# Performance work log

Measured on AMD Instinct MI355X. Metric: run time of the kernel, lower is better.

## Reference

```python
import jax, jax.numpy as jnp
import numpy as np

B, T, H = 32, 4096, 128   # batch, seq len, feature dim (ctor L=128)
N = 128                    # S5 state size (S5(dim, dim))
DEPTH = 2                  # L_LT
D_OUT = 64                 # adaptive pool output length (ctor D)
LN_EPS = 1e-5


def setup_inputs() -> dict:
    key = jax.random.key(0)
    ks = iter(jax.random.split(key, 40))
    def nrm(shape, s):
        return (jax.random.normal(next(ks), shape, jnp.float32) * s).astype(jnp.float32)
    inp = {}
    inp['x'] = jax.random.normal(next(ks), (B, T, H), jnp.float32)
    # LayerNorm params (stacked over depth)
    inp['ln1_g'] = jnp.ones((DEPTH, H), jnp.float32)
    inp['ln1_b'] = jnp.zeros((DEPTH, H), jnp.float32)
    inp['ln2_g'] = jnp.ones((DEPTH, H), jnp.float32)
    inp['ln2_b'] = jnp.zeros((DEPTH, H), jnp.float32)
    # S5 params: diagonal complex Lambda, complex B/C, real D skip, per-state log step
    inp['Lam_re'] = -0.5 * jnp.ones((DEPTH, N), jnp.float32)
    inp['Lam_im'] = jnp.tile(jnp.pi * jnp.arange(N, dtype=jnp.float32), (DEPTH, 1))
    inp['B_re'] = nrm((DEPTH, N, H), 1.0 / np.sqrt(H))
    inp['B_im'] = nrm((DEPTH, N, H), 1.0 / np.sqrt(H))
    inp['C_re'] = nrm((DEPTH, H, N), 1.0 / np.sqrt(N))
    inp['C_im'] = nrm((DEPTH, H, N), 1.0 / np.sqrt(N))
    inp['D_skip'] = nrm((DEPTH, H), 1.0)
    inp['log_step'] = jax.random.uniform(next(ks), (DEPTH, N), jnp.float32,
                                         minval=np.log(1e-3), maxval=np.log(1e-1))
    # MLP params
    inp['W1'] = nrm((DEPTH, H, 2 * H), 1.0 / np.sqrt(H))
    inp['b1'] = jnp.zeros((DEPTH, 2 * H), jnp.float32)
    inp['W2'] = nrm((DEPTH, 2 * H, H), 1.0 / np.sqrt(2 * H))
    inp['b2'] = jnp.zeros((DEPTH, H), jnp.float32)
    # Conv1d params (out_ch, in_ch, k=5)
    cs = 1.0 / np.sqrt(H * 5)
    inp['conv1_w'] = nrm((H, H, 5), cs)
    inp['conv1_b'] = jnp.zeros((H,), jnp.float32)
    inp['conv2_w'] = nrm((H, H, 5), cs)
    inp['conv2_b'] = jnp.zeros((H,), jnp.float32)
    return inp


def _layer_norm(x, g, b):
    mu = jnp.mean(x, axis=-1, keepdims=True)
    var = jnp.mean(jnp.square(x - mu), axis=-1, keepdims=True)
    return (x - mu) * jax.lax.rsqrt(var + LN_EPS) * g + b


def _s5(u, lam_re, lam_im, b_re, b_im, c_re, c_im, d_skip, log_step):
    # u: [B, T, H] real. Diagonal S5 with ZOH discretization + parallel scan.
    lam = lam_re + 1j * lam_im                       # (N,) complex
    dt = jnp.exp(log_step)                           # (N,)
    lam_bar = jnp.exp(lam * dt)                      # (N,)
    Bc = b_re + 1j * b_im                            # (N, H)
    B_bar = ((lam_bar - 1.0) / lam)[:, None] * Bc    # (N, H)
    Bu = jnp.einsum('bth,nh->btn', u.astype(jnp.complex64), B_bar)  # [B,T,N]
    A = jnp.broadcast_to(lam_bar.astype(jnp.complex64), Bu.shape)
    def binop(e1, e2):
        a1, x1 = e1
        a2, x2 = e2
        return a1 * a2, a2 * x1 + x2
    _, xs = jax.lax.associative_scan(binop, (A, Bu), axis=1)        # [B,T,N]
    Cc = c_re + 1j * c_im                            # (H, N)
    y = 2.0 * jnp.real(jnp.einsum('btn,hn->bth', xs, Cc)) + u * d_skip
    return y


def _conv1d_s2(x, w, b):
    # x: [B, C, L]; stride 2, padding 2, kernel 5
    y = jax.lax.conv_general_dilated(x, w, window_strides=(2,), padding=[(2, 2)],
                                     dimension_numbers=('NCH', 'OIH', 'NCH'))
    return y + b[None, :, None]


def reference(x, ln1_g, ln1_b, ln2_g, ln2_b, Lam_re, Lam_im, B_re, B_im,
              C_re, C_im, D_skip, log_step, W1, b1, W2, b2,
              conv1_w, conv1_b, conv2_w, conv2_b):
    for i in range(DEPTH):
        # S5 sub-block
        res = x
        xn = _layer_norm(x, ln1_g[i], ln1_b[i])
        x = res + _s5(xn, Lam_re[i], Lam_im[i], B_re[i], B_im[i],
                      C_re[i], C_im[i], D_skip[i], log_step[i])
        # MLP sub-block (dropout = identity in eval)
        res = x
        xn = _layer_norm(x, ln2_g[i], ln2_b[i])
        h = jax.nn.gelu(jnp.einsum('bth,hf->btf', xn, W1[i]) + b1[i], approximate=False)
        x = res + jnp.einsum('btf,fh->bth', h, W2[i]) + b2[i]
    x = jnp.transpose(x, (0, 2, 1))                  # [B, H, T]
    x = jax.nn.relu(_conv1d_s2(x, conv1_w, conv1_b))  # [B, H, T/2]
    x = jax.nn.relu(_conv1d_s2(x, conv2_w, conv2_b))  # [B, H, T/4]
    Lin = x.shape[-1]
    # AdaptiveAvgPool1d(D_OUT): Lin divisible by D_OUT -> uniform windows
    x = x.reshape(x.shape[0], x.shape[1], D_OUT, Lin // D_OUT).mean(axis=-1)
    return x  # [B, H, D_OUT]
```

## Files before the change

### kernel.cpp

```cpp
#include <hip/hip_runtime.h>
#include <math.h>

#define BATCH 32
#define TSEQ  4096
#define HD    128
#define NST   128
#define BT    (BATCH*TSEQ)
#define LC    64
#define NCHK  (TSEQ/LC)

typedef unsigned short bf16;
typedef __attribute__((ext_vector_type(8))) short bf16x8;
typedef __attribute__((ext_vector_type(4))) float f32x4;

__device__ inline float bf2f(bf16 s) {
    union { unsigned int u; float f; } v; v.u = ((unsigned int)s) << 16; return v.f;
}
__device__ inline bf16 f2bf(float f) {
    union { float f; unsigned int u; } v; v.f = f;
    unsigned int u = v.u;
    unsigned int r = (u + 0x7fffu + ((u >> 16) & 1u)) >> 16;
    return (bf16)r;
}
__device__ inline unsigned int pkpair(float lo, float hi) {
    union { float f; unsigned int u; } a, b;
    a.f = lo; b.f = hi;
    return __builtin_amdgcn_perm(b.u + 0x8000u, a.u + 0x8000u, 0x07060302u);
}
__device__ inline bf16x8 pack8f(float4 f0, float4 f1) {
    union { bf16x8 v; unsigned int u[4]; } t;
    t.u[0] = pkpair(f0.x, f0.y);
    t.u[1] = pkpair(f0.z, f0.w);
    t.u[2] = pkpair(f1.x, f1.y);
    t.u[3] = pkpair(f1.z, f1.w);
    return t.v;
}
__device__ inline float2 cmul2(float2 a, float2 b) {
    return make_float2(a.x*b.x - a.y*b.y, a.x*b.y + a.y*b.x);
}
__device__ inline float gelu_f(float x) {
    float u = x*(0.7978845608f + 0.0356774081f*x*x);
    return __fdividef(x, 1.f + __expf(-2.f*u));
}
__device__ inline float2 upk(unsigned int w) {
    union { unsigned int u; float f; } a, b;
    a.u = w << 16; b.u = w & 0xffff0000u;
    return make_float2(a.f, b.f);
}
__device__ inline unsigned int pk(float2 x) { return pkpair(x.x, x.y); }

__global__ void prep_s5(const float* __restrict__ Lam_re, const float* __restrict__ Lam_im,
                        const float* __restrict__ B_re,  const float* __restrict__ B_im,
                        const float* __restrict__ C_re,  const float* __restrict__ C_im,
                        const float* __restrict__ log_step,
                        const float* __restrict__ ln1_g, const float* __restrict__ ln1_b,
                        const float* __restrict__ D_skip,
                        bf16* __restrict__ Wbu_bf,
                        bf16* __restrict__ Wc_bf,
                        float* __restrict__ Sb, float* __restrict__ biasb,
                        float* __restrict__ gd, float* __restrict__ bd,
                        float4* __restrict__ coefs,
                        float2* __restrict__ apow)
{
    int i = blockIdx.x, n = threadIdx.x;
    int in = i*NST + n;
    float lr = Lam_re[in], li = Lam_im[in];
    float dt = expf(log_step[in]);
    float ea = expf(lr*dt);
    float ar = ea*cosf(li*dt), ai = ea*sinf(li*dt);
    float xx = ar - 1.f, yy = ai;
    float den = lr*lr + li*li;
    float sr = (xx*lr + yy*li)/den;
    float si = (yy*lr - xx*li)/den;
    float2 a2 = make_float2(ar, ai);
    float2 p = a2;
    float2* apr = apow + (size_t)i*64*128;
    for (int j = 0; j < 64; ++j) {
        apr[j*128 + n] = p;
        p = cmul2(p, a2);
    }
    float2 q = a2;
    #pragma unroll
    for (int t = 0; t < 6; ++t) q = cmul2(q, q);
    coefs[in] = make_float4(ar, ai, q.x, q.y);

    const float* g  = ln1_g + i*HD;
    const float* bb = ln1_b + i*HD;
    const float* br = B_re + (size_t)in*HD;
    const float* bi = B_im + (size_t)in*HD;
    bf16* wb = Wbu_bf + (size_t)i*256*128;
    float s_re = 0.f, s_im = 0.f, bc_re = 0.f, bc_im = 0.f;
    for (int h = 0; h < HD; ++h) {
        float wre = sr*br[h] - si*bi[h];
        float wim = sr*bi[h] + si*br[h];
        bf16 wrb = f2bf(g[h]*wre), wib = f2bf(g[h]*wim);
        wb[(2*n)*128 + h]   = wrb;
        wb[(2*n+1)*128 + h] = wib;
        s_re += bf2f(wrb); s_im += bf2f(wib);
        bc_re += bb[h]*wre; bc_im += bb[h]*wim;
    }
    Sb[i*256 + 2*n] = s_re;     Sb[i*256 + 2*n+1] = s_im;
    biasb[i*256 + 2*n] = bc_re; biasb[i*256 + 2*n+1] = bc_im;

    const float* cr = C_re + (size_t)i*HD*NST;
    const float* ci = C_im + (size_t)i*HD*NST;
    bf16* wc = Wc_bf + (size_t)i*128*256;
    for (int h = 0; h < HD; ++h) {
        wc[h*256 + 2*n]   = f2bf( 2.f * cr[h*NST + n]);
        wc[h*256 + 2*n+1] = f2bf(-2.f * ci[h*NST + n]);
    }
    gd[i*HD + n] = g[n]*D_skip[i*HD + n];
    bd[i*HD + n] = bb[n]*D_skip[i*HD + n];
}

__global__ void prep_w1(const float* __restrict__ W1, const float* __restrict__ b1,
                        const float* __restrict__ ln2_g, const float* __restrict__ ln2_b,
                        bf16* __restrict__ W1_bf, float* __restrict__ S1,
                        float* __restrict__ bias1p)
{
    int i = blockIdx.x, f = threadIdx.x;
    const float* g  = ln2_g + i*HD;
    const float* bb = ln2_b + i*HD;
    bf16* w = W1_bf + (size_t)i*256*128;
    float S = 0.f, bi_ = b1[i*256 + f];
    for (int h = 0; h < HD; ++h) {
        float wv = W1[(size_t)i*32768 + h*256 + f];
        bf16 wbv = f2bf(g[h]*wv);
        w[f*128 + h] = wbv;
        S += bf2f(wbv);
        bi_ += bb[h]*wv;
    }
    S1[i*256 + f] = S;
    bias1p[i*256 + f] = bi_;
}

__global__ void prep_w2(const float* __restrict__ W2, bf16* __restrict__ W2_bf)
{
    int i = blockIdx.x, h = threadIdx.x;
    bf16* w = W2_bf + (size_t)i*128*256;
    for (int f = 0; f < 256; ++f)
        w[h*256 + f] = f2bf(W2[(size_t)i*32768 + f*128 + h]);
}

__global__ void prep_wB(const float* __restrict__ w1, const float* __restrict__ w2,
                        bf16* __restrict__ wB1, bf16* __restrict__ wB2)
{
    int idx = blockIdx.x*256 + threadIdx.x;
    if (idx >= 163840) return;
    const float* w = (idx < 81920) ? w1 : w2;
    bf16* wb       = (idx < 81920) ? wB1 : wB2;
    int r   = idx % 81920;
    int c   = r / 640;
    int tap = (r % 640) / 128;
    int ic  = r % 128;
    wb[r] = f2bf(w[(c*128 + ic)*5 + tap]);
}

template<int UD, typename TA>
__global__ __launch_bounds__(1024, 4) void lngemm(
    const TA* __restrict__ A,
    const bf16* __restrict__ Bt,
    const float* __restrict__ Svec, const float* __restrict__ bvec,
    bf16* __restrict__ outB,
    float2* __restrict__ munrs)
{
    __shared__ bf16 Bs[256*136];
    __shared__ float Sl[256], bl[256];

    int tid = threadIdx.x;
    #pragma unroll
    for (int it = 0; it < 4; ++it) {
        int f = it*1024 + tid;
        int n = f >> 4, kk = (f & 15)*8;
        *(bf16x8*)&Bs[n*136 + kk] = *(const bf16x8*)(Bt + n*128 + kk);
    }
    if (tid < 256) { Sl[tid] = Svec[tid]; bl[tid] = bvec[tid]; }
    __syncthreads();

    int wid = tid >> 6, lane = tid & 63;
    int quad = lane >> 4, cl = lane & 15;
    int s = blockIdx.x*16 + wid;
    size_t row = (size_t)s*16 + cl;

    bf16x8 af[4];
    float sm = 0.f, sq = 0.f;
    if constexpr (sizeof(TA) == 2) {
        const bf16* ar = (const bf16*)A + row*128;
        #pragma unroll
        for (int ks = 0; ks < 4; ++ks) {
            af[ks] = *(const bf16x8*)(ar + quad*8 + ks*32);
            union { bf16x8 v; unsigned int u[4]; } aa; aa.v = af[ks];
            #pragma unroll
            for (int jp = 0; jp < 4; ++jp) {
                float2 vv = upk(aa.u[jp]);
                sm += vv.x + vv.y;
                sq += vv.x*vv.x + vv.y*vv.y;
            }
        }
    } else {
        const float* ar = (const float*)A + row*128;
        #pragma unroll
        for (int ks = 0; ks < 4; ++ks) {
            float4 f0 = *(const float4*)(ar + quad*8 + ks*32);
            float4 f1 = *(const float4*)(ar + quad*8 + ks*32 + 4);
            sm += f0.x + f0.y + f0.z + f0.w + f1.x + f1.y + f1.z + f1.w;
            sq += f0.x*f0.x + f0.y*f0.y + f0.z*f0.z + f0.w*f0.w
                + f1.x*f1.x + f1.y*f1.y + f1.z*f1.z + f1.w*f1.w;
            af[ks] = pack8f(f0, f1);
        }
    }
    sm += __shfl_xor(sm, 16); sm += __shfl_xor(sm, 32);
    sq += __shfl_xor(sq, 16); sq += __shfl_xor(sq, 32);
    float mu = sm * (1.f/128.f);
    float rs = rsqrtf(sq*(1.f/128.f) - mu*mu + 1e-5f);
    float mr = mu*rs;

    if constexpr (UD) {
        if (quad == 0) munrs[row] = make_float2(mu, rs);
    }

    #pragma unroll
    for (int half = 0; half < 2; ++half) {
        f32x4 acc[8] = {};
        #pragma unroll
        for (int nt = 0; nt < 8; ++nt) {
            const bf16* wrp = &Bs[((half*8+nt)*16 + cl)*136 + quad*8];
            #pragma unroll
            for (int ks = 0; ks < 4; ++ks)
                acc[nt] = __builtin_amdgcn_mfma_f32_16x16x32_bf16(
                              *(const bf16x8*)(wrp + ks*32), af[ks], acc[nt], 0, 0, 0);
        }
        #pragma unroll
        for (int nt = 0; nt < 8; ++nt) {
            int n0 = (half*8+nt)*16 + quad*4;
            float4 S4 = *(const float4*)&Sl[n0];
            float4 b4 = *(const float4*)&bl[n0];
            float4 o;
            o.x = rs*acc[nt][0] - mr*S4.x + b4.x;
            o.y = rs*acc[nt][1] - mr*S4.y + b4.y;
            o.z = rs*acc[nt][2] - mr*S4.z + b4.z;
            o.w = rs*acc[nt][3] - mr*S4.w + b4.w;
            if constexpr (!UD) {
                o.x = gelu_f(o.x); o.y = gelu_f(o.y);
                o.z = gelu_f(o.z); o.w = gelu_f(o.w);
            }
            uint2 pu = make_uint2(pkpair(o.x, o.y), pkpair(o.z, o.w));
            *(uint2*)(outB + row*256 + n0) = pu;
        }
    }
}

template<int EPI, typename TR>
__global__ __launch_bounds__(1024, 4) void gemm2(
    const bf16* __restrict__ A,
    const bf16* __restrict__ Bt,
    bf16* out,
    const float* __restrict__ bias,
    const TR* resid,
    const float2* __restrict__ munrs,
    const float* __restrict__ gdp, const float* __restrict__ bdp,
    const float2* __restrict__ carry,
    const float2* __restrict__ apow)
{
    __shared__ bf16 Bs[128*264];
    __shared__ float gdl[128], bdl[128];

    int tid = threadIdx.x;
    #pragma unroll
    for (int it = 0; it < 4; ++it) {
        int f = it*1024 + tid;
        int n = f >> 5, kk = (f & 31)*8;
        *(bf16x8*)&Bs[n*264 + kk] = *(const bf16x8*)(Bt + n*256 + kk);
    }
    if constexpr (EPI == 3) {
        if (tid < 128) { gdl[tid] = gdp[tid]; bdl[tid] = bdp[tid]; }
    } else {
        if (tid < 128) { gdl[tid] = bias[tid]; }
    }
    __syncthreads();

    int wid = tid >> 6, lane = tid & 63;
    int quad = lane >> 4, cl = lane & 15;
    int s = blockIdx.x*16 + wid;
    size_t row = (size_t)s*16 + cl;

    float mu = 0.f, rs = 0.f;
    if constexpr (EPI == 3) { float2 m2 = munrs[row]; mu = m2.x; rs = m2.y; }

    bf16x8 af[8];
    const bf16* ar = A + row*256 + quad*8;
    if constexpr (EPI == 3) {
        int b  = (int)(row >> 12);
        int tp = (int)(row & 4095);
        int cc = tp >> 6, j = tp & 63;
        const float2* cin = carry + (size_t)cc*(BATCH*NST) + (size_t)b*NST;
        const float2* ap  = apow + (size_t)j*128;
        #pragma unroll
        for (int ks = 0; ks < 8; ++ks) {
            union { bf16x8 v; unsigned int u[4]; } t;
            t.v = *(const bf16x8*)(ar + ks*32);
            int n0 = quad*4 + ks*16;
            #pragma unroll
            for (int jp = 0; jp < 4; ++jp) {
                float2 v  = upk(t.u[jp]);
                float2 ad = cmul2(ap[n0+jp], cin[n0+jp]);
                t.u[jp] = pk(make_float2(v.x + ad.x, v.y + ad.y));
            }
            af[ks] = t.v;
        }
    } else {
        #pragma unroll
        for (int ks = 0; ks < 8; ++ks)
            af[ks] = *(const bf16x8*)(ar + ks*32);
    }

    f32x4 acc[8] = {};
    #pragma unroll
    for (int nt = 0; nt < 8; ++nt) {
        const bf16* wrp = &Bs[(nt*16 + cl)*264 + quad*8];
        #pragma unroll
        for (int ks = 0; ks < 8; ++ks)
            acc[nt] = __builtin_amdgcn_mfma_f32_16x16x32_bf16(
                          *(const bf16x8*)(wrp + ks*32), af[ks], acc[nt], 0, 0, 0);
    }

    #pragma unroll
    for (int nt = 0; nt < 8; ++nt) {
        int n0 = nt*16 + quad*4;
        size_t oidx = row*128 + n0;
        float4 rv;
        if constexpr (sizeof(TR) == 2) {
            ushort4 u4 = *(const ushort4*)((const bf16*)resid + oidx);
            rv = make_float4(bf2f(u4.x), bf2f(u4.y), bf2f(u4.z), bf2f(u4.w));
        } else {
            rv = *(const float4*)((const float*)resid + oidx);
        }
        float4 o;
        if constexpr (EPI == 2) {
            float4 bv = *(const float4*)&gdl[n0];
            o.x = acc[nt][0] + bv.x + rv.x; o.y = acc[nt][1] + bv.y + rv.y;
            o.z = acc[nt][2] + bv.z + rv.z; o.w = acc[nt][3] + bv.w + rv.w;
        } else {
            float4 g4 = *(const float4*)&gdl[n0];
            float4 b4 = *(const float4*)&bdl[n0];
            o.x = rv.x + acc[nt][0] + (rv.x - mu)*rs*g4.x + b4.x;
            o.y = rv.y + acc[nt][1] + (rv.y - mu)*rs*g4.y + b4.y;
            o.z = rv.z + acc[nt][2] + (rv.z - mu)*rs*g4.z + b4.z;
            o.w = rv.w + acc[nt][3] + (rv.w - mu)*rs*g4.w + b4.w;
        }
        uint2 pu = make_uint2(pkpair(o.x, o.y), pkpair(o.z, o.w));
        *(uint2*)(out + oidx) = pu;
    }
}

__global__ __launch_bounds__(256) void scan_local(unsigned int* __restrict__ xs,
                                                  const float4* __restrict__ coefs,
                                                  float2* __restrict__ carry)
{
    int flat = blockIdx.x*256 + threadIdx.x;
    int n = flat & 127;
    int b = (flat >> 7) & 31;
    int c = flat >> 12;
    float4 cf = coefs[n];
    float2 a = make_float2(cf.x, cf.y);
    unsigned int* base = xs + ((size_t)(b*TSEQ + c*LC))*NST + n;
    float2 x = make_float2(0.f, 0.f);
    for (int j = 0; j < LC; ++j) {
        float2 v = upk(base[(size_t)j*NST]);
        x = make_float2(a.x*x.x - a.y*x.y + v.x, a.x*x.y + a.y*x.x + v.y);
        base[(size_t)j*NST] = pk(x);
    }
    carry[c*(BATCH*NST) + b*NST + n] = x;
}

__global__ void scan_carry(float2* __restrict__ carry, const float4* __restrict__ coefs)
{
    int flat = blockIdx.x*256 + threadIdx.x;
    int n = flat & 127;
    float4 cf = coefs[n];
    float2 aL = make_float2(cf.z, cf.w);
    float2 x = make_float2(0.f, 0.f);
    for (int c = 0; c < NCHK; ++c) {
        float2* p = carry + c*(BATCH*NST) + flat;
        float2 v = *p;
        *p = x;
        x = make_float2(aL.x*x.x - aL.y*x.y + v.x, aL.x*x.y + aL.y*x.x + v.y);
    }
}

__global__ __launch_bounds__(256, 4) void conv1_mfma(
    const bf16* __restrict__ X,
    const bf16* __restrict__ wB,
    const float* __restrict__ bias,
    bf16* __restrict__ out,
    int Tin, int Lout)
{
    __shared__ bf16 As[128][72];
    __shared__ bf16 Bs[128][72];
    int tid  = threadIdx.x;
    int lane = tid & 63;
    int wave = tid >> 6;
    int wm = wave >> 1, wn = wave & 1;
    int quad = lane >> 4, cl = lane & 15;
    int row0 = blockIdx.x * 128;
    int b  = row0 / Lout;
    int l0 = row0 % Lout;
    const bf16* Xb = X + (size_t)b*Tin*128;

    f32x4 acc[4][4] = {};

    for (int k0 = 0; k0 < 640; k0 += 64) {
        int tap = k0 / 128;
        int icb = k0 % 128;
        #pragma unroll
        for (int it = 0; it < 4; ++it) {
            int idx = it*256 + tid;
            int r = idx >> 3, kof = (idx & 7) * 8;
            int t = 2*(l0 + r) - 2 + tap;
            bf16x8 z = {0,0,0,0,0,0,0,0};
            if (t >= 0 && t < Tin) z = *(const bf16x8*)(Xb + (size_t)t*128 + icb + kof);
            *(bf16x8*)&As[r][kof] = z;
        }
        #pragma unroll
        for (int it = 0; it < 4; ++it) {
            int idx = it*256 + tid;
            int n = idx >> 3, kof = (idx & 7) * 8;
            *(bf16x8*)&Bs[n][kof] = *(const bf16x8*)(wB + (size_t)n*640 + k0 + kof);
        }
        __syncthreads();
        #pragma unroll
        for (int kk = 0; kk < 64; kk += 32) {
            bf16x8 af[4], bfr[4];
            #pragma unroll
            for (int i = 0; i < 4; ++i)
                af[i] = *(const bf16x8*)&As[wm*64 + i*16 + cl][kk + quad*8];
            #pragma unroll
            for (int j = 0; j < 4; ++j)
                bfr[j] = *(const bf16x8*)&Bs[wn*64 + j*16 + cl][kk + quad*8];
            #pragma unroll
            for (int i = 0; i < 4; ++i)
                #pragma unroll
                for (int j = 0; j < 4; ++j)
                    acc[i][j] = __builtin_amdgcn_mfma_f32_16x16x32_bf16(
                                    bfr[j], af[i], acc[i][j], 0, 0, 0);
        }
        __syncthreads();
    }

    #pragma unroll
    for (int i = 0; i < 4; ++i) {
        int grow = row0 + wm*64 + i*16 + cl;
        #pragma unroll
        for (int j = 0; j < 4; ++j) {
            int gcol = wn*64 + j*16 + quad*4;
            float4 bv = *(const float4*)(bias + gcol);
            float4 t;
            t.x = fmaxf(acc[i][j][0] + bv.x, 0.f); t.y = fmaxf(acc[i][j][1] + bv.y, 0.f);
            t.z = fmaxf(acc[i][j][2] + bv.z, 0.f); t.w = fmaxf(acc[i][j][3] + bv.w, 0.f);
            uint2 pu = make_uint2(pkpair(t.x, t.y), pkpair(t.z, t.w));
            *(uint2*)(out + (size_t)grow*128 + gcol) = pu;
        }
    }
}

__global__ __launch_bounds__(256, 4) void conv2_pool(
    const bf16* __restrict__ X,
    const bf16* __restrict__ wB,
    const float* __restrict__ bias,
    float* __restrict__ outp,
    int Tin, int Lout)
{
    __shared__ bf16 As[128][72];
    __shared__ bf16 Bs[128][72];
    int tid  = threadIdx.x;
    int lane = tid & 63;
    int wave = tid >> 6;
    int wm = wave >> 1, wn = wave & 1;
    int quad = lane >> 4, cl = lane & 15;
    int row0 = blockIdx.x * 128;
    int b  = row0 / Lout;
    int l0 = row0 % Lout;
    int d0 = l0 / 16;
    const bf16* Xb = X + (size_t)b*Tin*128;

    f32x4 acc[4][4] = {};

    for (int k0 = 0; k0 < 640; k0 += 64) {
        int tap = k0 / 128;
        int icb = k0 % 128;
        #pragma unroll
        for (int it = 0; it < 4; ++it) {
            int idx = it*256 + tid;
            int r = idx >> 3, kof = (idx & 7) * 8;
            int t = 2*(l0 + r) - 2 + tap;
            bf16x8 z = {0,0,0,0,0,0,0,0};
            if (t >= 0 && t < Tin) z = *(const bf16x8*)(Xb + (size_t)t*128 + icb + kof);
            *(bf16x8*)&As[r][kof] = z;
        }
        #pragma unroll
        for (int it = 0; it < 4; ++it) {
            int idx = it*256 + tid;
            int n = idx >> 3, kof = (idx & 7) * 8;
            *(bf16x8*)&Bs[n][kof] = *(const bf16x8*)(wB + (size_t)n*640 + k0 + kof);
        }
        __syncthreads();
        #pragma unroll
        for (int kk = 0; kk < 64; kk += 32) {
            bf16x8 af[4], bfr[4];
            #pragma unroll
            for (int i = 0; i < 4; ++i)
                af[i] = *(const bf16x8*)&As[wm*64 + i*16 + cl][kk + quad*8];
            #pragma unroll
            for (int j = 0; j < 4; ++j)
                bfr[j] = *(const bf16x8*)&Bs[wn*64 + j*16 + cl][kk + quad*8];
            #pragma unroll
            for (int i = 0; i < 4; ++i)
                #pragma unroll
                for (int j = 0; j < 4; ++j)
                    acc[i][j] = __builtin_amdgcn_mfma_f32_16x16x32_bf16(
                                    bfr[j], af[i], acc[i][j], 0, 0, 0);
        }
        __syncthreads();
    }

    #pragma unroll
    for (int j = 0; j < 4; ++j) {
        int gcol = wn*64 + j*16 + quad*4;
        float4 bv = *(const float4*)(bias + gcol);
        #pragma unroll
        for (int i = 0; i < 4; ++i) {
            float4 sp;
            sp.x = fmaxf(acc[i][j][0] + bv.x, 0.f);
            sp.y = fmaxf(acc[i][j][1] + bv.y, 0.f);
            sp.z = fmaxf(acc[i][j][2] + bv.z, 0.f);
            sp.w = fmaxf(acc[i][j][3] + bv.w, 0.f);
            #pragma unroll
            for (int off = 1; off <= 8; off <<= 1) {
                sp.x += __shfl_xor(sp.x, off);
                sp.y += __shfl_xor(sp.y, off);
                sp.z += __shfl_xor(sp.z, off);
                sp.w += __shfl_xor(sp.w, off);
            }
            if (cl == 0) {
                int d = d0 + wm*4 + i;
                float* op = outp + (size_t)b*8192 + (size_t)gcol*64 + d;
                op[0]   = sp.x * (1.f/16.f);
                op[64]  = sp.y * (1.f/16.f);
                op[128] = sp.z * (1.f/16.f);
                op[192] = sp.w * (1.f/16.f);
            }
        }
    }
}

extern "C" void kernel_launch(void* const* d_in, const int* in_sizes, int n_in,
                              void* d_out, int out_size, void* d_ws, size_t ws_size,
                              hipStream_t stream)
{
    (void)in_sizes; (void)n_in; (void)out_size; (void)ws_size;
    const float* x_in    = (const float*)d_in[0];
    const float* ln1_g   = (const float*)d_in[1];
    const float* ln1_b   = (const float*)d_in[2];
    const float* ln2_g   = (const float*)d_in[3];
    const float* ln2_b   = (const float*)d_in[4];
    const float* Lam_re  = (const float*)d_in[5];
    const float* Lam_im  = (const float*)d_in[6];
    const float* B_re    = (const float*)d_in[7];
    const float* B_im    = (const float*)d_in[8];
    const float* C_re    = (const float*)d_in[9];
    const float* C_im    = (const float*)d_in[10];
    const float* D_skip  = (const float*)d_in[11];
    const float* log_step= (const float*)d_in[12];
    const float* W1      = (const float*)d_in[13];
    const float* b1      = (const float*)d_in[14];
    const float* W2      = (const float*)d_in[15];
    const float* b2      = (const float*)d_in[16];
    const float* conv1_w = (const float*)d_in[17];
    const float* conv1_b = (const float*)d_in[18];
    const float* conv2_w = (const float*)d_in[19];
    const float* conv2_b = (const float*)d_in[20];
    float* out = (float*)d_out;

    char* ws = (char*)d_ws;
    bf16*   Xbf    = (bf16*) (ws);
    bf16*   Cbuf   = (bf16*) (ws + (size_t)33554432);
    bf16*   Cv1    = (bf16*) (ws + (size_t)100663296);
    float2* munrs  = (float2*)(ws + (size_t)117440512);
    char*   wreg   = ws + (size_t)118489088;
    bf16*   Wbu_bf = (bf16*)(wreg);
    bf16*   Wc_bf  = (bf16*)(wreg + 131072);
    bf16*   W1_bf  = (bf16*)(wreg + 262144);
    bf16*   W2_bf  = (bf16*)(wreg + 393216);
    float*  Sb     = (float*)(wreg + 524288);
    float*  biasb  = (float*)(wreg + 526336);
    float*  S1     = (float*)(wreg + 528384);
    float*  bias1p = (float*)(wreg + 530432);
    float*  gd     = (float*)(wreg + 532480);
    float*  bd     = (float*)(wreg + 533504);
    float4* coefs  = (float4*)(wreg + 534528);
    bf16*   wB1    = (bf16*)(wreg + 538624);
    bf16*   wB2    = (bf16*)(wreg + 702464);
    float2* carry  = (float2*)(wreg + 866304);
    float2* apow   = (float2*)(wreg + 2963456);

    prep_s5<<<2, 128, 0, stream>>>(Lam_re, Lam_im, B_re, B_im, C_re, C_im, log_step,
                                   ln1_g, ln1_b, D_skip,
                                   Wbu_bf, Wc_bf, Sb, biasb, gd, bd, coefs, apow);
    prep_w1<<<2, 256, 0, stream>>>(W1, b1, ln2_g, ln2_b, W1_bf, S1, bias1p);
    prep_w2<<<2, 128, 0, stream>>>(W2, W2_bf);
    prep_wB<<<640, 256, 0, stream>>>(conv1_w, conv2_w, wB1, wB2);

    for (int i = 0; i < 2; ++i) {
        if (i == 0)
            lngemm<1, float><<<512, 1024, 0, stream>>>(
                x_in, Wbu_bf, Sb, biasb, Cbuf, munrs);
        else
            lngemm<1, bf16><<<512, 1024, 0, stream>>>(
                Xbf, Wbu_bf + 32768, Sb + 256, biasb + 256, Cbuf, munrs);
        scan_local<<<1024, 256, 0, stream>>>((unsigned int*)Cbuf, coefs + i*NST, carry);
        scan_carry<<<16, 256, 0, stream>>>(carry, coefs + i*NST);
        if (i == 0)
            gemm2<3, float><<<512, 1024, 0, stream>>>(
                Cbuf, Wc_bf, Xbf, nullptr, x_in, munrs, gd, bd,
                carry, apow);
        else
            gemm2<3, bf16><<<512, 1024, 0, stream>>>(
                Cbuf, Wc_bf + 32768, Xbf, nullptr, Xbf, munrs, gd + 128, bd + 128,
                carry, apow + 64*128);
        lngemm<0, bf16><<<512, 1024, 0, stream>>>(
            Xbf, W1_bf + (size_t)i*32768, S1 + i*256, bias1p + i*256, Cbuf, nullptr);
        gemm2<2, bf16><<<512, 1024, 0, stream>>>(
            Cbuf, W2_bf + (size_t)i*32768, Xbf, b2 + i*HD, Xbf,
            nullptr, nullptr, nullptr, nullptr, nullptr);
    }

    conv1_mfma<<<512, 256, 0, stream>>>(Xbf, wB1, conv1_b, Cv1, 4096, 2048);
    conv2_pool<<<256, 256, 0, stream>>>(Cv1, wB2, conv2_b, out, 2048, 1024);
}
```

Before: 571.8 us.

## Fuse MLP up-projection, GELU and down-projection into one kernel

Replaces the separate LN+W1 GEMM and W2 GEMM launches with a single kernel that keeps the GELU hidden activations in registers and rearranges them across lanes with shuffles to form the second MFMA operand. This removes the write and re-read of the 256-wide hidden tensor through global memory, plus one launch per layer. Both weight matrices are staged in LDS, about 135KB per block, and the per-thread register load is high, so occupancy may drop to one block per CU despite the launch bound of two.

```diff
diff --git a/kernel.cpp b/kernel.cpp
--- a/kernel.cpp
+++ b/kernel.cpp
@@ -348,6 +348,140 @@
             o.z = rv.z + acc[nt][2] + (rv.z - mu)*rs*g4.z + b4.z;
             o.w = rv.w + acc[nt][3] + (rv.w - mu)*rs*g4.w + b4.w;
         }
+        uint2 pu = make_uint2(pkpair(o.x, o.y), pkpair(o.z, o.w));
+        *(uint2*)(out + oidx) = pu;
+    }
+}
+
+__global__ __launch_bounds__(1024, 2) void mlp_fused(
+    const bf16* X,
+    const bf16* __restrict__ W1t,
+    const bf16* __restrict__ W2t,
+    const float* __restrict__ S1v, const float* __restrict__ b1v,
+    const float* __restrict__ b2v,
+    bf16* out)
+{
+    __shared__ bf16 As1[256*136];
+    __shared__ bf16 Bs2[128*264];
+    __shared__ float S1l[256], b1l[256], b2l[128];
+
+    int tid = threadIdx.x;
+    #pragma unroll
+    for (int it = 0; it < 4; ++it) {
+        int f = it*1024 + tid;
+        int n = f >> 4, kk = (f & 15)*8;
+        *(bf16x8*)&As1[n*136 + kk] = *(const bf16x8*)(W1t + n*128 + kk);
+    }
+    #pragma unroll
+    for (int it = 0; it < 4; ++it) {
+        int f = it*1024 + tid;
+        int n = f >> 5, kk = (f & 31)*8;
+        *(bf16x8*)&Bs2[n*264 + kk] = *(const bf16x8*)(W2t + n*256 + kk);
+    }
+    if (tid < 256)      { S1l[tid] = S1v[tid]; b1l[tid] = b1v[tid]; }
+    else if (tid < 384) { int h = tid - 256; b2l[h] = b2v[h]; }
+    __syncthreads();
+
+    int wid = tid >> 6, lane = tid & 63;
+    int quad = lane >> 4, cl = lane & 15;
+    int s = blockIdx.x*16 + wid;
+    size_t row = (size_t)s*16 + cl;
+
+    bf16x8 af[4];
+    float sm = 0.f, sq = 0.f;
+    const bf16* ar = X + row*128;
+    #pragma unroll
+    for (int ks = 0; ks < 4; ++ks) {
+        af[ks] = *(const bf16x8*)(ar + quad*8 + ks*32);
+        union { bf16x8 v; unsigned int u[4]; } aa; aa.v = af[ks];
+        #pragma unroll
+        for (int jp = 0; jp < 4; ++jp) {
+            float2 vv = upk(aa.u[jp]);
+            sm += vv.x + vv.y;
+            sq += vv.x*vv.x + vv.y*vv.y;
+        }
+    }
+    ushort4 rvu[8];
+    #pragma unroll
+    for (int nt = 0; nt < 8; ++nt)
+        rvu[nt] = *(const ushort4*)(X + row*128 + nt*16 + quad*4);
+
+    sm += __shfl_xor(sm, 16); sm += __shfl_xor(sm, 32);
+    sq += __shfl_xor(sq, 16); sq += __shfl_xor(sq, 32);
+    float mu = sm * (1.f/128.f);
+    float rs = rsqrtf(sq*(1.f/128.f) - mu*mu + 1e-5f);
+    float mr = mu*rs;
+
+    unsigned int hp[16][2];
+    #pragma unroll
+    for (int half = 0; half < 2; ++half) {
+        f32x4 acc[8] = {};
+        #pragma unroll
+        for (int nt = 0; nt < 8; ++nt) {
+            const bf16* wrp = &As1[((half*8+nt)*16 + cl)*136 + quad*8];
+            #pragma unroll
+            for (int ks = 0; ks < 4; ++ks)
+                acc[nt] = __builtin_amdgcn_mfma_f32_16x16x32_bf16(
+                              *(const bf16x8*)(wrp + ks*32), af[ks], acc[nt], 0, 0, 0);
+        }
+        #pragma unroll
+        for (int nt = 0; nt < 8; ++nt) {
+            int NT = half*8 + nt;
+            int n0 = NT*16 + quad*4;
+            float4 S4 = *(const float4*)&S1l[n0];
+            float4 b4 = *(const float4*)&b1l[n0];
+            float4 o;
+            o.x = gelu_f(rs*acc[nt][0] - mr*S4.x + b4.x);
+            o.y = gelu_f(rs*acc[nt][1] - mr*S4.y + b4.y);
+            o.z = gelu_f(rs*acc[nt][2] - mr*S4.z + b4.z);
+            o.w = gelu_f(rs*acc[nt][3] - mr*S4.w + b4.w);
+            hp[NT][0] = pkpair(o.x, o.y);
+            hp[NT][1] = pkpair(o.z, o.w);
+        }
+    }
+
+    bf16x8 af2[8];
+    int sl0 = (((quad & 1) << 1) << 4) + cl;
+    int sl1 = sl0 + 16;
+    int hi = quad >> 1;
+    #pragma unroll
+    for (int ks = 0; ks < 8; ++ks) {
+        unsigned int a0 = (unsigned int)__shfl((int)hp[2*ks][0],   sl0, 64);
+        unsigned int a1 = (unsigned int)__shfl((int)hp[2*ks][1],   sl0, 64);
+        unsigned int a2 = (unsigned int)__shfl((int)hp[2*ks][0],   sl1, 64);
+        unsigned int a3 = (unsigned int)__shfl((int)hp[2*ks][1],   sl1, 64);
+        unsigned int c0 = (unsigned int)__shfl((int)hp[2*ks+1][0], sl0, 64);
+        unsigned int c1 = (unsigned int)__shfl((int)hp[2*ks+1][1], sl0, 64);
+        unsigned int c2 = (unsigned int)__shfl((int)hp[2*ks+1][0], sl1, 64);
+        unsigned int c3 = (unsigned int)__shfl((int)hp[2*ks+1][1], sl1, 64);
+        union { bf16x8 v; unsigned int u[4]; } t;
+        t.u[0] = hi ? c0 : a0;
+        t.u[1] = hi ? c1 : a1;
+        t.u[2] = hi ? c2 : a2;
+        t.u[3] = hi ? c3 : a3;
+        af2[ks] = t.v;
+    }
+
+    f32x4 acc2[8] = {};
+    #pragma unroll
+    for (int nt = 0; nt < 8; ++nt) {
+        const bf16* wrp = &Bs2[(nt*16 + cl)*264 + quad*8];
+        #pragma unroll
+        for (int ks = 0; ks < 8; ++ks)
+            acc2[nt] = __builtin_amdgcn_mfma_f32_16x16x32_bf16(
+                           *(const bf16x8*)(wrp + ks*32), af2[ks], acc2[nt], 0, 0, 0);
+    }
+
+    #pragma unroll
+    for (int nt = 0; nt < 8; ++nt) {
+        int n0 = nt*16 + quad*4;
+        size_t oidx = row*128 + n0;
+        float4 b4 = *(const float4*)&b2l[n0];
+        float4 o;
+        o.x = acc2[nt][0] + b4.x + bf2f(rvu[nt].x);
+        o.y = acc2[nt][1] + b4.y + bf2f(rvu[nt].y);
+        o.z = acc2[nt][2] + b4.z + bf2f(rvu[nt].z);
+        o.w = acc2[nt][3] + b4.w + bf2f(rvu[nt].w);
         uint2 pu = make_uint2(pkpair(o.x, o.y), pkpair(o.z, o.w));
         *(uint2*)(out + oidx) = pu;
     }
@@ -627,11 +761,9 @@
             gemm2<3, bf16><<<512, 1024, 0, stream>>>(
                 Cbuf, Wc_bf + 32768, Xbf, nullptr, Xbf, munrs, gd + 128, bd + 128,
                 carry, apow + 64*128);
-        lngemm<0, bf16><<<512, 1024, 0, stream>>>(
-            Xbf, W1_bf + (size_t)i*32768, S1 + i*256, bias1p + i*256, Cbuf, nullptr);
-        gemm2<2, bf16><<<512, 1024, 0, stream>>>(
-            Cbuf, W2_bf + (size_t)i*32768, Xbf, b2 + i*HD, Xbf,
-            nullptr, nullptr, nullptr, nullptr, nullptr);
+        mlp_fused<<<512, 1024, 0, stream>>>(
+            Xbf, W1_bf + (size_t)i*32768, W2_bf + (size_t)i*32768,
+            S1 + i*256, bias1p + i*256, b2 + i*HD, Xbf);
     }
 
     conv1_mfma<<<512, 256, 0, stream>>>(Xbf, wB1, conv1_b, Cv1, 4096, 2048);
```

Result: faster. 548.6 us (-4.1%).

## Fuse MLP GEMMs into one kernel and process two row tiles per wave

Applied to the files above, without the earlier changes.

The two MLP GEMMs (LN+W1+GELU and W2+residual) become a single kernel that keeps the GELU hidden activations in registers as the A operand of the second GEMM. This removes the 256-wide intermediate write and read through global memory. W1 rows are permuted at prep time so the MFMA output layout matches the input fragment layout of the second MFMA. The S5 projection kernels now handle two 16-row tiles per wave with 512-thread blocks, reusing each LDS weight fragment across two MFMAs, at the cost of more registers and lower occupancy.

```diff
diff --git a/kernel.cpp b/kernel.cpp
--- a/kernel.cpp
+++ b/kernel.cpp
@@ -122,11 +122,12 @@
     const float* g  = ln2_g + i*HD;
     const float* bb = ln2_b + i*HD;
     bf16* w = W1_bf + (size_t)i*256*128;
+    int j = ((f >> 5) << 5) | (((f >> 2) & 1) << 4) | (((f >> 3) & 3) << 2) | (f & 3);
     float S = 0.f, bi_ = b1[i*256 + f];
     for (int h = 0; h < HD; ++h) {
         float wv = W1[(size_t)i*32768 + h*256 + f];
         bf16 wbv = f2bf(g[h]*wv);
-        w[f*128 + h] = wbv;
+        w[j*128 + h] = wbv;
         S += bf2f(wbv);
         bi_ += bb[h]*wv;
     }
@@ -156,8 +157,8 @@
     wb[r] = f2bf(w[(c*128 + ic)*5 + tap]);
 }
 
-template<int UD, typename TA>
-__global__ __launch_bounds__(1024, 4) void lngemm(
+template<typename TA>
+__global__ __launch_bounds__(512, 2) void lngemm2(
     const TA* __restrict__ A,
     const bf16* __restrict__ Bt,
     const float* __restrict__ Svec, const float* __restrict__ bvec,
@@ -169,8 +170,8 @@
 
     int tid = threadIdx.x;
     #pragma unroll
-    for (int it = 0; it < 4; ++it) {
-        int f = it*1024 + tid;
+    for (int it = 0; it < 8; ++it) {
+        int f = it*512 + tid;
         int n = f >> 4, kk = (f & 15)*8;
         *(bf16x8*)&Bs[n*136 + kk] = *(const bf16x8*)(Bt + n*128 + kk);
     }
@@ -179,83 +180,86 @@
 
     int wid = tid >> 6, lane = tid & 63;
     int quad = lane >> 4, cl = lane & 15;
-    int s = blockIdx.x*16 + wid;
-    size_t row = (size_t)s*16 + cl;
-
-    bf16x8 af[4];
-    float sm = 0.f, sq = 0.f;
-    if constexpr (sizeof(TA) == 2) {
-        const bf16* ar = (const bf16*)A + row*128;
-        #pragma unroll
-        for (int ks = 0; ks < 4; ++ks) {
-            af[ks] = *(const bf16x8*)(ar + quad*8 + ks*32);
-            union { bf16x8 v; unsigned int u[4]; } aa; aa.v = af[ks];
-            #pragma unroll
-            for (int jp = 0; jp < 4; ++jp) {
-                float2 vv = upk(aa.u[jp]);
-                sm += vv.x + vv.y;
-                sq += vv.x*vv.x + vv.y*vv.y;
-            }
-        }
-    } else {
-        const float* ar = (const float*)A + row*128;
-        #pragma unroll
-        for (int ks = 0; ks < 4; ++ks) {
-            float4 f0 = *(const float4*)(ar + quad*8 + ks*32);
-            float4 f1 = *(const float4*)(ar + quad*8 + ks*32 + 4);
-            sm += f0.x + f0.y + f0.z + f0.w + f1.x + f1.y + f1.z + f1.w;
-            sq += f0.x*f0.x + f0.y*f0.y + f0.z*f0.z + f0.w*f0.w
-                + f1.x*f1.x + f1.y*f1.y + f1.z*f1.z + f1.w*f1.w;
-            af[ks] = pack8f(f0, f1);
-        }
-    }
-    sm += __shfl_xor(sm, 16); sm += __shfl_xor(sm, 32);
-    sq += __shfl_xor(sq, 16); sq += __shfl_xor(sq, 32);
-    float mu = sm * (1.f/128.f);
-    float rs = rsqrtf(sq*(1.f/128.f) - mu*mu + 1e-5f);
-    float mr = mu*rs;
-
-    if constexpr (UD) {
-        if (quad == 0) munrs[row] = make_float2(mu, rs);
-    }
-
-    #pragma unroll
-    for (int half = 0; half < 2; ++half) {
-        f32x4 acc[8] = {};
-        #pragma unroll
-        for (int nt = 0; nt < 8; ++nt) {
-            const bf16* wrp = &Bs[((half*8+nt)*16 + cl)*136 + quad*8];
-            #pragma unroll
-            for (int ks = 0; ks < 4; ++ks)
-                acc[nt] = __builtin_amdgcn_mfma_f32_16x16x32_bf16(
-                              *(const bf16x8*)(wrp + ks*32), af[ks], acc[nt], 0, 0, 0);
-        }
-        #pragma unroll
-        for (int nt = 0; nt < 8; ++nt) {
-            int n0 = (half*8+nt)*16 + quad*4;
+    int s0 = blockIdx.x*16 + wid*2;
+    size_t row0 = (size_t)s0*16 + cl;
+
+    bf16x8 af[2][4];
+    float mu[2], rs[2], mr[2];
+    #pragma unroll
+    for (int p = 0; p < 2; ++p) {
+        size_t row = row0 + (size_t)p*16;
+        float sm = 0.f, sq = 0.f;
+        if constexpr (sizeof(TA) == 2) {
+            const bf16* ar = (const bf16*)A + row*128;
+            #pragma unroll
+            for (int ks = 0; ks < 4; ++ks) {
+                af[p][ks] = *(const bf16x8*)(ar + quad*8 + ks*32);
+                union { bf16x8 v; unsigned int u[4]; } aa; aa.v = af[p][ks];
+                #pragma unroll
+                for (int jp = 0; jp < 4; ++jp) {
+                    float2 vv = upk(aa.u[jp]);
+                    sm += vv.x + vv.y;
+                    sq += vv.x*vv.x + vv.y*vv.y;
+                }
+            }
+        } else {
+            const float* ar = (const float*)A + row*128;
+            #pragma unroll
+            for (int ks = 0; ks < 4; ++ks) {
+                float4 f0 = *(const float4*)(ar + quad*8 + ks*32);
+                float4 f1 = *(const float4*)(ar + quad*8 + ks*32 + 4);
+                sm += f0.x + f0.y + f0.z + f0.w + f1.x + f1.y + f1.z + f1.w;
+                sq += f0.x*f0.x + f0.y*f0.y + f0.z*f0.z + f0.w*f0.w
+                    + f1.x*f1.x + f1.y*f1.y + f1.z*f1.z + f1.w*f1.w;
+                af[p][ks] = pack8f(f0, f1);
+            }
+        }
+        sm += __shfl_xor(sm, 16); sm += __shfl_xor(sm, 32);
+        sq += __shfl_xor(sq, 16); sq += __shfl_xor(sq, 32);
+        mu[p] = sm * (1.f/128.f);
+        rs[p] = rsqrtf(sq*(1.f/128.f) - mu[p]*mu[p] + 1e-5f);
+        mr[p] = mu[p]*rs[p];
+        if (quad == 0) munrs[row] = make_float2(mu[p], rs[p]);
+    }
+
+    #pragma unroll
+    for (int g = 0; g < 4; ++g) {
+        f32x4 acc0[4] = {}, acc1[4] = {};
+        #pragma unroll
+        for (int t4 = 0; t4 < 4; ++t4) {
+            const bf16* wrp = &Bs[(((g*4+t4)*16) + cl)*136 + quad*8];
+            #pragma unroll
+            for (int ks = 0; ks < 4; ++ks) {
+                bf16x8 w = *(const bf16x8*)(wrp + ks*32);
+                acc0[t4] = __builtin_amdgcn_mfma_f32_16x16x32_bf16(w, af[0][ks], acc0[t4], 0, 0, 0);
+                acc1[t4] = __builtin_amdgcn_mfma_f32_16x16x32_bf16(w, af[1][ks], acc1[t4], 0, 0, 0);
+            }
+        }
+        #pragma unroll
+        for (int t4 = 0; t4 < 4; ++t4) {
+            int n0 = (g*4+t4)*16 + quad*4;
             float4 S4 = *(const float4*)&Sl[n0];
             float4 b4 = *(const float4*)&bl[n0];
             float4 o;
-            o.x = rs*acc[nt][0] - mr*S4.x + b4.x;
-            o.y = rs*acc[nt][1] - mr*S4.y + b4.y;
-            o.z = rs*acc[nt][2] - mr*S4.z + b4.z;
-            o.w = rs*acc[nt][3] - mr*S4.w + b4.w;
-            if constexpr (!UD) {
-                o.x = gelu_f(o.x); o.y = gelu_f(o.y);
-                o.z = gelu_f(o.z); o.w = gelu_f(o.w);
-            }
-            uint2 pu = make_uint2(pkpair(o.x, o.y), pkpair(o.z, o.w));
-            *(uint2*)(outB + row*256 + n0) = pu;
-        }
-    }
-}
-
-template<int EPI, typename TR>
-__global__ __launch_bounds__(1024, 4) void gemm2(
+            o.x = rs[0]*acc0[t4][0] - mr[0]*S4.x + b4.x;
+            o.y = rs[0]*acc0[t4][1] - mr[0]*S4.y + b4.y;
+            o.z = rs[0]*acc0[t4][2] - mr[0]*S4.z + b4.z;
+            o.w = rs[0]*acc0[t4][3] - mr[0]*S4.w + b4.w;
+            *(uint2*)(outB + row0*256 + n0) = make_uint2(pkpair(o.x, o.y), pkpair(o.z, o.w));
+            o.x = rs[1]*acc1[t4][0] - mr[1]*S4.x + b4.x;
+            o.y = rs[1]*acc1[t4][1] - mr[1]*S4.y + b4.y;
+            o.z = rs[1]*acc1[t4][2] - mr[1]*S4.z + b4.z;
+            o.w = rs[1]*acc1[t4][3] - mr[1]*S4.w + b4.w;
+            *(uint2*)(outB + (row0+16)*256 + n0) = make_uint2(pkpair(o.x, o.y), pkpair(o.z, o.w));
+        }
+    }
+}
+
+template<typename TR>
+__global__ __launch_bounds__(512, 2) void gemm2s(
     const bf16* __restrict__ A,
     const bf16* __restrict__ Bt,
     bf16* out,
-    const float* __restrict__ bias,
     const TR* resid,
     const float2* __restrict__ munrs,
     const float* __restrict__ gdp, const float* __restrict__ bdp,
@@ -267,29 +271,26 @@
 
     int tid = threadIdx.x;
     #pragma unroll
-    for (int it = 0; it < 4; ++it) {
-        int f = it*1024 + tid;
+    for (int it = 0; it < 8; ++it) {
+        int f = it*512 + tid;
         int n = f >> 5, kk = (f & 31)*8;
         *(bf16x8*)&Bs[n*264 + kk] = *(const bf16x8*)(Bt + n*256 + kk);
     }
-    if constexpr (EPI == 3) {
-        if (tid < 128) { gdl[tid] = gdp[tid]; bdl[tid] = bdp[tid]; }
-    } else {
-        if (tid < 128) { gdl[tid] = bias[tid]; }
-    }
+    if (tid < 128) { gdl[tid] = gdp[tid]; bdl[tid] = bdp[tid]; }
     __syncthreads();
 
     int wid = tid >> 6, lane = tid & 63;
     int quad = lane >> 4, cl = lane & 15;
-    int s = blockIdx.x*16 + wid;
-    size_t row = (size_t)s*16 + cl;
-
-    float mu = 0.f, rs = 0.f;
-    if constexpr (EPI == 3) { float2 m2 = munrs[row]; mu = m2.x; rs = m2.y; }
-
-    bf16x8 af[8];
-    const bf16* ar = A + row*256 + quad*8;
-    if constexpr (EPI == 3) {
+    int s0 = blockIdx.x*16 + wid*2;
+    size_t row0 = (size_t)s0*16 + cl;
+
+    bf16x8 af[2][8];
+    float mu[2], rs[2];
+    #pragma unroll
+    for (int p = 0; p < 2; ++p) {
+        size_t row = row0 + (size_t)p*16;
+        float2 m2 = munrs[row]; mu[p] = m2.x; rs[p] = m2.y;
+        const bf16* ar = A + row*256 + quad*8;
         int b  = (int)(row >> 12);
         int tp = (int)(row & 4095);
         int cc = tp >> 6, j = tp & 63;
@@ -306,50 +307,156 @@
                 float2 ad = cmul2(ap[n0+jp], cin[n0+jp]);
                 t.u[jp] = pk(make_float2(v.x + ad.x, v.y + ad.y));
             }
-            af[ks] = t.v;
-        }
-    } else {
-        #pragma unroll
-        for (int ks = 0; ks < 8; ++ks)
-            af[ks] = *(const bf16x8*)(ar + ks*32);
-    }
-
-    f32x4 acc[8] = {};
+            af[p][ks] = t.v;
+        }
+    }
+
     #pragma unroll
     for (int nt = 0; nt < 8; ++nt) {
         const bf16* wrp = &Bs[(nt*16 + cl)*264 + quad*8];
-        #pragma unroll
-        for (int ks = 0; ks < 8; ++ks)
-            acc[nt] = __builtin_amdgcn_mfma_f32_16x16x32_bf16(
-                          *(const bf16x8*)(wrp + ks*32), af[ks], acc[nt], 0, 0, 0);
+        f32x4 a0 = {}, a1 = {};
+        #pragma unroll
+        for (int ks = 0; ks < 8; ++ks) {
+            bf16x8 w = *(const bf16x8*)(wrp + ks*32);
+            a0 = __builtin_amdgcn_mfma_f32_16x16x32_bf16(w, af[0][ks], a0, 0, 0, 0);
+            a1 = __builtin_amdgcn_mfma_f32_16x16x32_bf16(w, af[1][ks], a1, 0, 0, 0);
+        }
+        int n0 = nt*16 + quad*4;
+        float4 g4 = *(const float4*)&gdl[n0];
+        float4 b4 = *(const float4*)&bdl[n0];
+        #pragma unroll
+        for (int p = 0; p < 2; ++p) {
+            f32x4 ac = p ? a1 : a0;
+            size_t oidx = (row0 + (size_t)p*16)*128 + n0;
+            float4 rv;
+            if constexpr (sizeof(TR) == 2) {
+                ushort4 u4 = *(const ushort4*)((const bf16*)resid + oidx);
+                rv = make_float4(bf2f(u4.x), bf2f(u4.y), bf2f(u4.z), bf2f(u4.w));
+            } else {
+                rv = *(const float4*)((const float*)resid + oidx);
+            }
+            float4 o;
+            o.x = rv.x + ac[0] + (rv.x - mu[p])*rs[p]*g4.x + b4.x;
+            o.y = rv.y + ac[1] + (rv.y - mu[p])*rs[p]*g4.y + b4.y;
+            o.z = rv.z + ac[2] + (rv.z - mu[p])*rs[p]*g4.z + b4.z;
+            o.w = rv.w + ac[3] + (rv.w - mu[p])*rs[p]*g4.w + b4.w;
+            *(uint2*)(out + oidx) = make_uint2(pkpair(o.x, o.y), pkpair(o.z, o.w));
+        }
+    }
+}
+
+__global__ __launch_bounds__(1024, 4) void mlp_fused(
+    const bf16* X,
+    const bf16* __restrict__ W1t,
+    const bf16* __restrict__ W2t,
+    const float* __restrict__ S1v, const float* __restrict__ b1v,
+    const float* __restrict__ b2v,
+    bf16* out)
+{
+    __shared__ bf16 As1[256*136];
+    __shared__ bf16 Bs2[128*264];
+    __shared__ float S1l[256], b1l[256], b2l[128];
+
+    int tid = threadIdx.x;
+    #pragma unroll
+    for (int it = 0; it < 4; ++it) {
+        int f = it*1024 + tid;
+        int n = f >> 4, kk = (f & 15)*8;
+        *(bf16x8*)&As1[n*136 + kk] = *(const bf16x8*)(W1t + n*128 + kk);
+    }
+    #pragma unroll
+    for (int it = 0; it < 4; ++it) {
+        int f = it*1024 + tid;
+        int n = f >> 5, kk = (f & 31)*8;
+        *(bf16x8*)&Bs2[n*264 + kk] = *(const bf16x8*)(W2t + n*256 + kk);
+    }
+    if (tid < 256)      { S1l[tid] = S1v[tid]; b1l[tid] = b1v[tid]; }
+    else if (tid < 384) { int h = tid - 256; b2l[h] = b2v[h]; }
+    __syncthreads();
+
+    int wid = tid >> 6, lane = tid & 63;
+    int quad = lane >> 4, cl = lane & 15;
+    int s0 = blockIdx.x*32 + wid*2;
+    size_t row0 = (size_t)s0*16 + cl;
+
+    typedef union { unsigned int u[16][2]; bf16x8 v[8]; } HP;
+    HP hpa[2];
+
+    #pragma unroll
+    for (int p = 0; p < 2; ++p) {
+        size_t row = row0 + (size_t)p*16;
+        const bf16* ar = X + row*128;
+        bf16x8 af[4];
+        float sm = 0.f, sq = 0.f;
+        #pragma unroll
+        for (int ks = 0; ks < 4; ++ks) {
+            af[ks] = *(const bf16x8*)(ar + quad*8 + ks*32);
+            union { bf16x8 v; unsigned int u[4]; } aa; aa.v = af[ks];
+            #pragma unroll
+            for (int jp = 0; jp < 4; ++jp) {
+                float2 vv = upk(aa.u[jp]);
+                sm += vv.x + vv.y;
+                sq += vv.x*vv.x + vv.y*vv.y;
+            }
+        }
+        sm += __shfl_xor(sm, 16); sm += __shfl_xor(sm, 32);
+        sq += __shfl_xor(sq, 16); sq += __shfl_xor(sq, 32);
+        float mu = sm * (1.f/128.f);
+        float rs = rsqrtf(sq*(1.f/128.f) - mu*mu + 1e-5f);
+        float mr = mu*rs;
+
+        #pragma unroll
+        for (int g = 0; g < 4; ++g) {
+            f32x4 acc[4] = {};
+            #pragma unroll
+            for (int t4 = 0; t4 < 4; ++t4) {
+                const bf16* wrp = &As1[(((g*4+t4)*16) + cl)*136 + quad*8];
+                #pragma unroll
+                for (int ks = 0; ks < 4; ++ks)
+                    acc[t4] = __builtin_amdgcn_mfma_f32_16x16x32_bf16(
+                                  *(const bf16x8*)(wrp + ks*32), af[ks], acc[t4], 0, 0, 0);
+            }
+            #pragma unroll
+            for (int t4 = 0; t4 < 4; ++t4) {
+                int NT = g*4 + t4;
+                int fb = ((NT >> 1) << 5) + (quad << 3) + ((NT & 1) << 2);
+                float4 S4 = *(const float4*)&S1l[fb];
+                float4 b4 = *(const float4*)&b1l[fb];
+                float4 o;
+                o.x = gelu_f(rs*acc[t4][0] - mr*S4.x + b4.x);
+                o.y = gelu_f(rs*acc[t4][1] - mr*S4.y + b4.y);
+                o.z = gelu_f(rs*acc[t4][2] - mr*S4.z + b4.z);
+                o.w = gelu_f(rs*acc[t4][3] - mr*S4.w + b4.w);
+                hpa[p].u[NT][0] = pkpair(o.x, o.y);
+                hpa[p].u[NT][1] = pkpair(o.z, o.w);
+            }
+        }
     }
 
     #pragma unroll
     for (int nt = 0; nt < 8; ++nt) {
+        const bf16* wrp = &Bs2[(nt*16 + cl)*264 + quad*8];
+        f32x4 a0 = {}, a1 = {};
+        #pragma unroll
+        for (int ks = 0; ks < 8; ++ks) {
+            bf16x8 w = *(const bf16x8*)(wrp + ks*32);
+            a0 = __builtin_amdgcn_mfma_f32_16x16x32_bf16(w, hpa[0].v[ks], a0, 0, 0, 0);
+            a1 = __builtin_amdgcn_mfma_f32_16x16x32_bf16(w, hpa[1].v[ks], a1, 0, 0, 0);
+        }
         int n0 = nt*16 + quad*4;
-        size_t oidx = row*128 + n0;
-        float4 rv;
-        if constexpr (sizeof(TR) == 2) {
-            ushort4 u4 = *(const ushort4*)((const bf16*)resid + oidx);
-            rv = make_float4(bf2f(u4.x), bf2f(u4.y), bf2f(u4.z), bf2f(u4.w));
-        } else {
-            rv = *(const float4*)((const float*)resid + oidx);
-        }
-        float4 o;
-        if constexpr (EPI == 2) {
-            float4 bv = *(const float4*)&gdl[n0];
-            o.x = acc[nt][0] + bv.x + rv.x; o.y = acc[nt][1] + bv.y + rv.y;
-            o.z = acc[nt][2] + bv.z + rv.z; o.w = acc[nt][3] + bv.w + rv.w;
-        } else {
-            float4 g4 = *(const float4*)&gdl[n0];
-            float4 b4 = *(const float4*)&bdl[n0];
-            o.x = rv.x + acc[nt][0] + (rv.x - mu)*rs*g4.x + b4.x;
-            o.y = rv.y + acc[nt][1] + (rv.y - mu)*rs*g4.y + b4.y;
-            o.z = rv.z + acc[nt][2] + (rv.z - mu)*rs*g4.z + b4.z;
-            o.w = rv.w + acc[nt][3] + (rv.w - mu)*rs*g4.w + b4.w;
-        }
-        uint2 pu = make_uint2(pkpair(o.x, o.y), pkpair(o.z, o.w));
-        *(uint2*)(out + oidx) = pu;
+        float4 b4 = *(const float4*)&b2l[n0];
+        #pragma unroll
+        for (int p = 0; p < 2; ++p) {
+            f32x4 ac = p ? a1 : a0;
+            size_t oidx = (row0 + (size_t)p*16)*128 + n0;
+            ushort4 u4 = *(const ushort4*)(X + oidx);
+            float4 o;
+            o.x = ac[0] + b4.x + bf2f(u4.x);
+            o.y = ac[1] + b4.y + bf2f(u4.y);
+            o.z = ac[2] + b4.z + bf2f(u4.z);
+            o.w = ac[3] + b4.w + bf2f(u4.w);
+            *(uint2*)(out + oidx) = make_uint2(pkpair(o.x, o.y), pkpair(o.z, o.w));
+        }
     }
 }
 
@@ -612,26 +719,23 @@
 
     for (int i = 0; i < 2; ++i) {
         if (i == 0)
-            lngemm<1, float><<<512, 1024, 0, stream>>>(
+            lngemm2<float><<<512, 512, 0, stream>>>(
                 x_in, Wbu_bf, Sb, biasb, Cbuf, munrs);
         else
-            lngemm<1, bf16><<<512, 1024, 0, stream>>>(
+            lngemm2<bf16><<<512, 512, 0, stream>>>(
                 Xbf, Wbu_bf + 32768, Sb + 256, biasb + 256, Cbuf, munrs);
         scan_local<<<1024, 256, 0, stream>>>((unsigned int*)Cbuf, coefs + i*NST, carry);
         scan_carry<<<16, 256, 0, stream>>>(carry, coefs + i*NST);
         if (i == 0)
-            gemm2<3, float><<<512, 1024, 0, stream>>>(
-                Cbuf, Wc_bf, Xbf, nullptr, x_in, munrs, gd, bd,
-                carry, apow);
+            gemm2s<float><<<512, 512, 0, stream>>>(
+                Cbuf, Wc_bf, Xbf, x_in, munrs, gd, bd, carry, apow);
         else
-            gemm2<3, bf16><<<512, 1024, 0, stream>>>(
-                Cbuf, Wc_bf + 32768, Xbf, nullptr, Xbf, munrs, gd + 128, bd + 128,
+            gemm2s<bf16><<<512, 512, 0, stream>>>(
+                Cbuf, Wc_bf + 32768, Xbf, Xbf, munrs, gd + 128, bd + 128,
                 carry, apow + 64*128);
-        lngemm<0, bf16><<<512, 1024, 0, stream>>>(
-            Xbf, W1_bf + (size_t)i*32768, S1 + i*256, bias1p + i*256, Cbuf, nullptr);
-        gemm2<2, bf16><<<512, 1024, 0, stream>>>(
-            Cbuf, W2_bf + (size_t)i*32768, Xbf, b2 + i*HD, Xbf,
-            nullptr, nullptr, nullptr, nullptr, nullptr);
+        mlp_fused<<<256, 1024, 0, stream>>>(
+            Xbf, W1_bf + (size_t)i*32768, W2_bf + (size_t)i*32768,
+            S1 + i*256, bias1p + i*256, b2 + i*HD, Xbf);
     }
 
     conv1_mfma<<<512, 256, 0, stream>>>(Xbf, wB1, conv1_b, Cv1, 4096, 2048);
```

After: 737.9 us. 1.29x slower.
